# Kernel tuning notes

Hardware: AMD Instinct MI355X
Metric: run time of the kernel (lower is better)

Reference implementation:

```python
import jax, jax.numpy as jnp
import numpy as np

EMBED = 2048
HEADS = 16
HEAD_DIM = EMBED // HEADS


def setup_inputs() -> dict:
    key = jax.random.key(0)
    ks = jax.random.split(key, 9)
    s = 1.0 / np.sqrt(EMBED)
    inp = {"x": jax.random.normal(ks[0], (2, 2048, EMBED), dtype=jnp.float32)}
    for i, name in enumerate(["q", "k", "v", "o"]):
        inp[f"W{name}"] = jax.random.uniform(ks[1 + 2 * i], (EMBED, EMBED), dtype=jnp.float32, minval=-s, maxval=s)
        inp[f"b{name}"] = jax.random.uniform(ks[2 + 2 * i], (EMBED,), dtype=jnp.float32, minval=-s, maxval=s)
    return inp


def reference(x, Wq, bq, Wk, bk, Wv, bv, Wo, bo):
    B, S, E = x.shape
    def split_heads(t):
        return t.reshape(B, S, HEADS, HEAD_DIM).transpose(0, 2, 1, 3)  # [B,H,S,D]
    q = split_heads(x @ Wq.T + bq)
    k = split_heads(x @ Wk.T + bk)
    v = split_heads(x @ Wv.T + bv)
    scale = 1.0 / np.sqrt(HEAD_DIM)
    scores = jnp.einsum("bhqd,bhkd->bhqk", q, k) * scale  # [B,H,S,S]
    causal = jnp.tril(jnp.ones((S, S), dtype=bool))
    scores = jnp.where(causal[None, None], scores, -jnp.inf)
    attn = jax.nn.softmax(scores, axis=-1)
    out = jnp.einsum("bhqk,bhkd->bhqd", attn, v)  # [B,H,S,D]
    out = out.transpose(0, 2, 1, 3).reshape(B, S, E)
    return out @ Wo.T + bo
```

## Files before the change

kernel.cpp:

```cpp
#include <hip/hip_runtime.h>

typedef unsigned short u16;
typedef unsigned int u32;
typedef __attribute__((ext_vector_type(8))) short bf16x8;
typedef __attribute__((ext_vector_type(4))) float f32x4;

#define MFMA(a, b, c) __builtin_amdgcn_mfma_f32_16x16x32_bf16((a), (b), (c), 0, 0, 0)

__device__ inline u16 f2bf(float f) {
  u32 u = __float_as_uint(f);
  u = (u + 0x7fffu + ((u >> 16) & 1u)) >> 16;
  return (u16)u;
}

__device__ inline void gld16(u16* lds, const u16* g) {
  __builtin_amdgcn_global_load_lds((const __attribute__((address_space(1))) void*)g,
                                   (__attribute__((address_space(3))) void*)lds,
                                   16, 0, 0);
}

__global__ __launch_bounds__(256) void cvt_all(const float* __restrict__ x,
                                               const float* __restrict__ wa,
                                               const float* __restrict__ wb,
                                               const float* __restrict__ wc,
                                               const float* __restrict__ wd,
                                               uint2* __restrict__ dst) {
  int i = blockIdx.x * 256 + threadIdx.x;
  const float* s;
  int off;
  if (i < 2097152) {
    s = x; off = i;
  } else {
    int j = i - 2097152;
    int which = j >> 20;
    off = j & 1048575;
    s = (which == 0) ? wa : (which == 1) ? wb : (which == 2) ? wc : wd;
  }
  float4 f = ((const float4*)s)[off];
  u32 lo = (u32)f2bf(f.x) | ((u32)f2bf(f.y) << 16);
  u32 hi = (u32)f2bf(f.z) | ((u32)f2bf(f.w) << 16);
  dst[i] = make_uint2(lo, hi);
}

__device__ inline void gemm_core(const u16* __restrict__ A, const u16* __restrict__ W,
                                 u16* As, u16* Bs, int m0, int n0, f32x4 acc[4][4]) {
  const int K = 2048;
  const int NT = 64;
  int t = threadIdx.x, w = t >> 6, l = t & 63;
  int wr = (w >> 1) * 64, wc = (w & 1) * 64;
  int fr = l & 15, fg = l >> 4;
  int r0 = t >> 2;
  int r1 = 64 + r0;
  int c00 = (t & 3) ^ ((r0 >> 1) & 3);
  int c01 = (t & 3) ^ ((r1 >> 1) & 3);
  const u16* gA = A + (size_t)m0 * K;
  const u16* gB = W + (size_t)n0 * K;
  size_t a0 = (size_t)r0 * K + c00 * 8;
  size_t a1 = (size_t)r1 * K + c01 * 8;
#pragma unroll
  for (int p = 0; p < 2; ++p) {
    u16* sa = As + p * 4096;
    u16* sb = Bs + p * 4096;
    int kk = p * 32;
    gld16(sa + w * 512, gA + a0 + kk);
    gld16(sa + 2048 + w * 512, gA + a1 + kk);
    gld16(sb + w * 512, gB + a0 + kk);
    gld16(sb + 2048 + w * 512, gB + a1 + kk);
  }
  for (int kt = 0; kt < NT; ++kt) {
    int kt2 = (kt + 2 < NT) ? (kt + 2) : (NT - 1);
    u16* sa = As + ((kt + 2) & 3) * 4096;
    u16* sb = Bs + ((kt + 2) & 3) * 4096;
    int kk = kt2 * 32;
    gld16(sa + w * 512, gA + a0 + kk);
    gld16(sa + 2048 + w * 512, gA + a1 + kk);
    gld16(sb + w * 512, gB + a0 + kk);
    gld16(sb + 2048 + w * 512, gB + a1 + kk);
    asm volatile("s_waitcnt vmcnt(8)\n\ts_barrier" ::: "memory");
    const u16* ca = As + (kt & 3) * 4096;
    const u16* cb = Bs + (kt & 3) * 4096;
    bf16x8 af[4], bfv[4];
#pragma unroll
    for (int i = 0; i < 4; ++i) {
      int ar = wr + i * 16 + fr;
      af[i] = *(const bf16x8*)&ca[ar * 32 + ((fg ^ ((ar >> 1) & 3)) << 3)];
    }
#pragma unroll
    for (int i = 0; i < 4; ++i) {
      int br = wc + i * 16 + fr;
      bfv[i] = *(const bf16x8*)&cb[br * 32 + ((fg ^ ((br >> 1) & 3)) << 3)];
    }
    __builtin_amdgcn_s_setprio(1);
#pragma unroll
    for (int mi = 0; mi < 4; ++mi)
#pragma unroll
      for (int ni = 0; ni < 4; ++ni)
        acc[mi][ni] = MFMA(af[mi], bfv[ni], acc[mi][ni]);
    __builtin_amdgcn_s_setprio(0);
  }
}

__global__ __launch_bounds__(512, 2) void qk_gemm(
    const u16* __restrict__ X, const u16* __restrict__ Wq, const u16* __restrict__ Wk,
    const float* __restrict__ bq, const float* __restrict__ bk, u16* __restrict__ Qo,
    u16* __restrict__ Ko) {
  __shared__ __attribute__((aligned(16))) u16 As[32768];
  __shared__ __attribute__((aligned(16))) u16 Bs[32768];
  const int K = 2048, NT = 64;
  int which = blockIdx.x >> 3;
  int n0 = (blockIdx.x & 7) * 256;
  int m0 = blockIdx.y * 256;
  const u16* W = (which == 0) ? Wq : Wk;
  const float* bias = (which == 0) ? bq : bk;
  u16* out = (which == 0) ? Qo : Ko;
  float scale = (which == 0) ? 0.08838834764831845f : 1.0f;
  int t = threadIdx.x, w = t >> 6, l = t & 63;
  int wm = w >> 2, wn = w & 3;
  int fr = l & 15, fg = l >> 4;
  int r0 = t >> 2;
  int c0 = (t & 3) ^ ((r0 >> 1) & 3);
  const u16* gA = X + (size_t)m0 * K;
  const u16* gB = W + (size_t)n0 * K;
  size_t a0 = (size_t)r0 * K + c0 * 8;
  size_t a1 = a0 + (size_t)128 * K;
  f32x4 zero4 = {0.f, 0.f, 0.f, 0.f};
  f32x4 acc[8][4];
#pragma unroll
  for (int i = 0; i < 8; ++i)
#pragma unroll
    for (int j = 0; j < 4; ++j) acc[i][j] = zero4;
#pragma unroll
  for (int p = 0; p < 2; ++p) {
    u16* sa = As + p * 8192;
    u16* sb = Bs + p * 8192;
    int kk = p * 32;
    gld16(sa + w * 512, gA + a0 + kk);
    gld16(sa + 4096 + w * 512, gA + a1 + kk);
    gld16(sb + w * 512, gB + a0 + kk);
    gld16(sb + 4096 + w * 512, gB + a1 + kk);
  }
  for (int kt = 0; kt < NT; ++kt) {
    int kt2 = (kt + 2 < NT) ? (kt + 2) : (NT - 1);
    u16* sa = As + ((kt + 2) & 3) * 8192;
    u16* sb = Bs + ((kt + 2) & 3) * 8192;
    int kk = kt2 * 32;
    gld16(sa + w * 512, gA + a0 + kk);
    gld16(sa + 4096 + w * 512, gA + a1 + kk);
    gld16(sb + w * 512, gB + a0 + kk);
    gld16(sb + 4096 + w * 512, gB + a1 + kk);
    asm volatile("s_waitcnt vmcnt(8)\n\ts_barrier" ::: "memory");
    const u16* ca = As + (kt & 3) * 8192;
    const u16* cb = Bs + (kt & 3) * 8192;
    bf16x8 af[8], bfv[4];
#pragma unroll
    for (int i = 0; i < 8; ++i) {
      int ar = wm * 128 + i * 16 + fr;
      af[i] = *(const bf16x8*)&ca[ar * 32 + ((fg ^ ((ar >> 1) & 3)) << 3)];
    }
#pragma unroll
    for (int i = 0; i < 4; ++i) {
      int br = wn * 64 + i * 16 + fr;
      bfv[i] = *(const bf16x8*)&cb[br * 32 + ((fg ^ ((br >> 1) & 3)) << 3)];
    }
    __builtin_amdgcn_s_setprio(1);
#pragma unroll
    for (int mi = 0; mi < 8; ++mi)
#pragma unroll
      for (int ni = 0; ni < 4; ++ni)
        acc[mi][ni] = MFMA(af[mi], bfv[ni], acc[mi][ni]);
    __builtin_amdgcn_s_setprio(0);
  }
#pragma unroll
  for (int mi = 0; mi < 8; ++mi) {
#pragma unroll
    for (int ni = 0; ni < 4; ++ni) {
      int row = m0 + wm * 128 + mi * 16 + (l >> 4) * 4;
      int col = n0 + wn * 64 + ni * 16 + (l & 15);
      float bb = bias[col];
      int h = col >> 7, d = col & 127;
#pragma unroll
      for (int i = 0; i < 4; ++i) {
        int m = row + i;
        int b = m >> 11, s = m & 2047;
        float v = (acc[mi][ni][i] + bb) * scale;
        out[(((size_t)b * 16 + h) * 2048 + s) * 128 + d] = f2bf(v);
      }
    }
  }
}

__global__ __launch_bounds__(256, 2) void v_gemm(const u16* __restrict__ X,
                                                 const u16* __restrict__ Wv,
                                                 const float* __restrict__ bv,
                                                 u16* __restrict__ Vo) {
  __shared__ __attribute__((aligned(16))) u16 As[16384];
  __shared__ __attribute__((aligned(16))) u16 Bs[16384];
  int n0 = blockIdx.x * 128, m0 = blockIdx.y * 128;
  f32x4 zero4 = {0.f, 0.f, 0.f, 0.f};
  f32x4 acc[4][4];
#pragma unroll
  for (int i = 0; i < 4; ++i)
#pragma unroll
    for (int j = 0; j < 4; ++j) acc[i][j] = zero4;
  gemm_core(X, Wv, As, Bs, m0, n0, acc);
  int t = threadIdx.x, w = t >> 6, l = t & 63;
  int wr = (w >> 1) * 64, wc = (w & 1) * 64;
#pragma unroll
  for (int mi = 0; mi < 4; ++mi) {
#pragma unroll
    for (int ni = 0; ni < 4; ++ni) {
      int row = m0 + wr + mi * 16 + (l >> 4) * 4;
      int col = n0 + wc + ni * 16 + (l & 15);
      float bb = bv[col];
      int h = col >> 7, d = col & 127;
      int b = row >> 11, s = row & 2047;
      u32 p0 = (u32)f2bf(acc[mi][ni][0] + bb) | ((u32)f2bf(acc[mi][ni][1] + bb) << 16);
      u32 p1 = (u32)f2bf(acc[mi][ni][2] + bb) | ((u32)f2bf(acc[mi][ni][3] + bb) << 16);
      *(uint2*)&Vo[((size_t)(b * 16 + h) * 128 + d) * 2048 + s] = make_uint2(p0, p1);
    }
  }
}

__global__ __launch_bounds__(256, 2) void oproj_gemm(const u16* __restrict__ A,
                                                     const u16* __restrict__ W,
                                                     const float* __restrict__ bias,
                                                     float* __restrict__ out) {
  __shared__ __attribute__((aligned(16))) u16 As[16384];
  __shared__ __attribute__((aligned(16))) u16 Bs[16384];
  int n0 = blockIdx.x * 128, m0 = blockIdx.y * 128;
  f32x4 zero4 = {0.f, 0.f, 0.f, 0.f};
  f32x4 acc[4][4];
#pragma unroll
  for (int i = 0; i < 4; ++i)
#pragma unroll
    for (int j = 0; j < 4; ++j) acc[i][j] = zero4;
  gemm_core(A, W, As, Bs, m0, n0, acc);
  int t = threadIdx.x, w = t >> 6, l = t & 63;
  int wr = (w >> 1) * 64, wc = (w & 1) * 64;
#pragma unroll
  for (int mi = 0; mi < 4; ++mi) {
#pragma unroll
    for (int ni = 0; ni < 4; ++ni) {
      int row = m0 + wr + mi * 16 + (l >> 4) * 4;
      int col = n0 + wc + ni * 16 + (l & 15);
      float bb = bias[col];
#pragma unroll
      for (int i = 0; i < 4; ++i) out[(size_t)(row + i) * 2048 + col] = acc[mi][ni][i] + bb;
    }
  }
}

__global__ __launch_bounds__(512, 4) void attn_fwd(const u16* __restrict__ Q,
                                                   const u16* __restrict__ K,
                                                   const u16* __restrict__ Vt,
                                                   u16* __restrict__ AO) {
  __shared__ __attribute__((aligned(16))) u16 Ks[16384];
  __shared__ __attribute__((aligned(16))) u16 Vts[16384];
  __shared__ __attribute__((aligned(16))) u16 Pl[8192];
  const int D = 128;
  int b3 = blockIdx.x;
  int bh = b3 & 31;
  int xq = b3 >> 5;
  int qt = (xq < 8) ? (15 - xq) : (xq - 8);
  int t = threadIdx.x, w = t >> 6, l = t & 63, g = l >> 4, c = l & 15;
  size_t base = (size_t)bh * 2048 * 128;
  const u16* Vbh = Vt + base;
  int q0 = qt * 128;
  int qrw = q0 + w * 16;
  bf16x8 qf[4];
  {
    const u16* qp = Q + base + (size_t)(qrw + c) * D + g * 8;
#pragma unroll
    for (int ks = 0; ks < 4; ++ks) qf[ks] = *(const bf16x8*)(qp + ks * 32);
  }
  f32x4 zero4 = {0.f, 0.f, 0.f, 0.f};
  f32x4 oacc[8];
#pragma unroll
  for (int i = 0; i < 8; ++i) oacc[i] = zero4;
  f32x4 lacc = zero4;
  bf16x8 ones;
#pragma unroll
  for (int i = 0; i < 8; ++i) ones[i] = (short)0x3F80;
  float mrow[4];
#pragma unroll
  for (int i = 0; i < 4; ++i) mrow[i] = -1e30f;
  char* pw = (char*)(Pl + w * 1024);
  int ktmax = 2 * qt + 1;
#define STAGE_TILE(BUF, KV0)                                                          \
  {                                                                                   \
    _Pragma("unroll") for (int i = 0; i < 2; ++i) {                                   \
      int row = i * 32 + w * 4 + (l >> 4);                                            \
      int cc = (l & 15) ^ (row & 7);                                                  \
      gld16(Ks + (BUF)*8192 + i * 4096 + w * 512,                                     \
            K + base + (size_t)((KV0) + row) * D + cc * 8);                           \
    }                                                                                 \
    _Pragma("unroll") for (int i = 0; i < 2; ++i) {                                   \
      int vr = i * 64 + w * 8 + (l >> 3);                                             \
      int vslot = (l & 7) ^ ((l >> 3) & 7);                                           \
      gld16(Vts + (BUF)*8192 + i * 4096 + w * 512,                                    \
            Vbh + (size_t)vr * 2048 + (KV0) + vslot * 8);                             \
    }                                                                                 \
  }
  STAGE_TILE(0, 0)
  for (int kt = 0; kt <= ktmax; ++kt) {
    int kv0 = kt * 64;
    int ktn = (kt + 1 <= ktmax) ? (kt + 1) : ktmax;
    STAGE_TILE((kt + 1) & 1, ktn * 64)
    asm volatile("s_waitcnt vmcnt(4)\n\ts_barrier" ::: "memory");
    const u16* Kb = Ks + (kt & 1) * 8192;
    const u16* Vb2 = Vts + (kt & 1) * 8192;
    if (kv0 <= qrw + 15) {
      f32x4 sacc[4];
#pragma unroll
      for (int n = 0; n < 4; ++n) sacc[n] = zero4;
#pragma unroll
      for (int ks = 0; ks < 4; ++ks) {
#pragma unroll
        for (int n = 0; n < 4; ++n) {
          int row = n * 16 + c;
          bf16x8 kf = *(const bf16x8*)&Kb[row * 128 + (((ks * 4 + g) ^ (c & 7)) << 3)];
          sacc[n] = MFMA(qf[ks], kf, sacc[n]);
        }
      }
      float sc[4][4];
#pragma unroll
      for (int n = 0; n < 4; ++n)
#pragma unroll
        for (int i = 0; i < 4; ++i) sc[n][i] = sacc[n][i];
      if (kv0 + 63 > qrw) {
#pragma unroll
        for (int n = 0; n < 4; ++n) {
          int kv = kv0 + n * 16 + c;
#pragma unroll
          for (int i = 0; i < 4; ++i)
            if (kv > qrw + g * 4 + i) sc[n][i] = -1e30f;
        }
      }
      float tmax[4];
#pragma unroll
      for (int i = 0; i < 4; ++i)
        tmax[i] = fmaxf(fmaxf(sc[0][i], sc[1][i]), fmaxf(sc[2][i], sc[3][i]));
#pragma unroll
      for (int x = 1; x < 16; x <<= 1)
#pragma unroll
        for (int i = 0; i < 4; ++i) tmax[i] = fmaxf(tmax[i], __shfl_xor(tmax[i], x));
      float corr[4];
#pragma unroll
      for (int i = 0; i < 4; ++i) {
        float mn = fmaxf(mrow[i], tmax[i]);
        corr[i] = __expf(mrow[i] - mn);
        mrow[i] = mn;
      }
#pragma unroll
      for (int i = 0; i < 4; ++i) lacc[i] *= corr[i];
#pragma unroll
      for (int nf = 0; nf < 8; ++nf)
#pragma unroll
        for (int i = 0; i < 4; ++i) oacc[nf][i] *= corr[i];
      float ps[4][4];
#pragma unroll
      for (int n = 0; n < 4; ++n)
#pragma unroll
        for (int i = 0; i < 4; ++i) ps[n][i] = __expf(sc[n][i] - mrow[i]);
#pragma unroll
      for (int n = 0; n < 4; ++n)
#pragma unroll
        for (int i = 0; i < 4; ++i) {
          int row = g * 4 + i;
          *(u16*)(pw + row * 128 + ((n * 32 + c * 2) ^ ((row & 7) << 4))) = f2bf(ps[n][i]);
        }
#pragma unroll
      for (int ks = 0; ks < 2; ++ks) {
        bf16x8 pf = *(const bf16x8*)(pw + c * 128 + ((ks * 64 + g * 16) ^ ((c & 7) << 4)));
        lacc = MFMA(pf, ones, lacc);
#pragma unroll
        for (int nf = 0; nf < 8; ++nf) {
          bf16x8 vf = *(const bf16x8*)&Vb2[(nf * 16 + c) * 64 + (((ks * 4 + g) ^ (c & 7)) << 3)];
          oacc[nf] = MFMA(pf, vf, oacc[nf]);
        }
      }
    }
    __syncthreads();
  }
  int b = bh >> 4, h = bh & 15;
#pragma unroll
  for (int nf = 0; nf < 8; ++nf) {
    int d = h * 128 + nf * 16 + c;
#pragma unroll
    for (int i = 0; i < 4; ++i) {
      int q = qrw + g * 4 + i;
      AO[((size_t)b * 2048 + q) * 2048 + d] = f2bf(oacc[nf][i] / lacc[i]);
    }
  }
}

extern "C" void kernel_launch(void* const* d_in, const int* in_sizes, int n_in,
                              void* d_out, int out_size, void* d_ws, size_t ws_size,
                              hipStream_t stream) {
  const float* x = (const float*)d_in[0];
  const float* Wq = (const float*)d_in[1];
  const float* bq = (const float*)d_in[2];
  const float* Wk = (const float*)d_in[3];
  const float* bk = (const float*)d_in[4];
  const float* Wv = (const float*)d_in[5];
  const float* bv = (const float*)d_in[6];
  const float* Wo = (const float*)d_in[7];
  const float* bo = (const float*)d_in[8];
  float* out = (float*)d_out;

  u16* xb = (u16*)d_ws;
  u16* Wqb = xb + 8388608;
  u16* Wkb = Wqb + 4194304;
  u16* Wvb = Wkb + 4194304;
  u16* Wob = Wvb + 4194304;
  u16* Qb = Wob + 4194304;
  u16* Kb = Qb + 8388608;
  u16* Vb = Kb + 8388608;
  u16* AOb = xb;

  cvt_all<<<24576, 256, 0, stream>>>(x, Wq, Wk, Wv, Wo, (uint2*)d_ws);
  qk_gemm<<<dim3(16, 16), 512, 0, stream>>>(xb, Wqb, Wkb, bq, bk, Qb, Kb);
  v_gemm<<<dim3(16, 32), 256, 0, stream>>>(xb, Wvb, bv, Vb);
  attn_fwd<<<512, 512, 0, stream>>>(Qb, Kb, Vb, AOb);
  oproj_gemm<<<dim3(16, 32), 256, 0, stream>>>(AOb, Wob, bo, out);
}
```

Baseline: 259.1 us.

## Use single-buffered 128-wide KV tiles in attention instead of double-buffered 64

The attention loop now stages 128-key K and V tiles into the whole LDS region, replacing two alternating 64-key buffers. This halves the number of loop iterations, barriers and online-softmax rescales per key. In exchange it drops prefetching of the next tile, so global loads no longer overlap with MFMA work and each iteration waits for all loads. The P matrix is written and consumed in two halves to reuse the per-warp P buffer.

```diff
diff --git a/kernel.cpp b/kernel.cpp
--- a/kernel.cpp
+++ b/kernel.cpp
@@ -285,51 +285,44 @@
 #pragma unroll
   for (int i = 0; i < 4; ++i) mrow[i] = -1e30f;
   char* pw = (char*)(Pl + w * 1024);
-  int ktmax = 2 * qt + 1;
-#define STAGE_TILE(BUF, KV0)                                                          \
-  {                                                                                   \
-    _Pragma("unroll") for (int i = 0; i < 2; ++i) {                                   \
-      int row = i * 32 + w * 4 + (l >> 4);                                            \
-      int cc = (l & 15) ^ (row & 7);                                                  \
-      gld16(Ks + (BUF)*8192 + i * 4096 + w * 512,                                     \
-            K + base + (size_t)((KV0) + row) * D + cc * 8);                           \
-    }                                                                                 \
-    _Pragma("unroll") for (int i = 0; i < 2; ++i) {                                   \
-      int vr = i * 64 + w * 8 + (l >> 3);                                             \
-      int vslot = (l & 7) ^ ((l >> 3) & 7);                                           \
-      gld16(Vts + (BUF)*8192 + i * 4096 + w * 512,                                    \
-            Vbh + (size_t)vr * 2048 + (KV0) + vslot * 8);                             \
-    }                                                                                 \
-  }
-  STAGE_TILE(0, 0)
-  for (int kt = 0; kt <= ktmax; ++kt) {
-    int kv0 = kt * 64;
-    int ktn = (kt + 1 <= ktmax) ? (kt + 1) : ktmax;
-    STAGE_TILE((kt + 1) & 1, ktn * 64)
-    asm volatile("s_waitcnt vmcnt(4)\n\ts_barrier" ::: "memory");
-    const u16* Kb = Ks + (kt & 1) * 8192;
-    const u16* Vb2 = Vts + (kt & 1) * 8192;
+  for (int kt = 0; kt <= qt; ++kt) {
+    int kv0 = kt * 128;
+    __syncthreads();
+#pragma unroll
+    for (int i = 0; i < 4; ++i) {
+      int row = i * 32 + w * 4 + (l >> 4);
+      int cc = (l & 15) ^ (row & 7);
+      gld16(Ks + i * 4096 + w * 512, K + base + (size_t)(kv0 + row) * D + cc * 8);
+    }
+#pragma unroll
+    for (int i = 0; i < 4; ++i) {
+      int vr = i * 32 + w * 4 + (l >> 4);
+      int cc = (l & 15) ^ (vr & 7);
+      gld16(Vts + i * 4096 + w * 512, Vbh + (size_t)vr * 2048 + kv0 + cc * 8);
+    }
+    asm volatile("s_waitcnt vmcnt(0)" ::: "memory");
+    __syncthreads();
     if (kv0 <= qrw + 15) {
-      f32x4 sacc[4];
-#pragma unroll
-      for (int n = 0; n < 4; ++n) sacc[n] = zero4;
+      f32x4 sacc[8];
+#pragma unroll
+      for (int n = 0; n < 8; ++n) sacc[n] = zero4;
 #pragma unroll
       for (int ks = 0; ks < 4; ++ks) {
 #pragma unroll
-        for (int n = 0; n < 4; ++n) {
+        for (int n = 0; n < 8; ++n) {
           int row = n * 16 + c;
-          bf16x8 kf = *(const bf16x8*)&Kb[row * 128 + (((ks * 4 + g) ^ (c & 7)) << 3)];
+          bf16x8 kf = *(const bf16x8*)&Ks[row * 128 + (((ks * 4 + g) ^ (c & 7)) << 3)];
           sacc[n] = MFMA(qf[ks], kf, sacc[n]);
         }
       }
-      float sc[4][4];
-#pragma unroll
-      for (int n = 0; n < 4; ++n)
+      float sc[8][4];
+#pragma unroll
+      for (int n = 0; n < 8; ++n)
 #pragma unroll
         for (int i = 0; i < 4; ++i) sc[n][i] = sacc[n][i];
-      if (kv0 + 63 > qrw) {
-#pragma unroll
-        for (int n = 0; n < 4; ++n) {
+      if (kv0 + 127 > qrw) {
+#pragma unroll
+        for (int n = 0; n < 8; ++n) {
           int kv = kv0 + n * 16 + c;
 #pragma unroll
           for (int i = 0; i < 4; ++i)
@@ -338,8 +331,11 @@
       }
       float tmax[4];
 #pragma unroll
-      for (int i = 0; i < 4; ++i)
-        tmax[i] = fmaxf(fmaxf(sc[0][i], sc[1][i]), fmaxf(sc[2][i], sc[3][i]));
+      for (int i = 0; i < 4; ++i) {
+        float m01 = fmaxf(sc[0][i], sc[1][i]), m23 = fmaxf(sc[2][i], sc[3][i]);
+        float m45 = fmaxf(sc[4][i], sc[5][i]), m67 = fmaxf(sc[6][i], sc[7][i]);
+        tmax[i] = fmaxf(fmaxf(m01, m23), fmaxf(m45, m67));
+      }
 #pragma unroll
       for (int x = 1; x < 16; x <<= 1)
 #pragma unroll
@@ -357,30 +353,34 @@
       for (int nf = 0; nf < 8; ++nf)
 #pragma unroll
         for (int i = 0; i < 4; ++i) oacc[nf][i] *= corr[i];
-      float ps[4][4];
-#pragma unroll
-      for (int n = 0; n < 4; ++n)
-#pragma unroll
-        for (int i = 0; i < 4; ++i) ps[n][i] = __expf(sc[n][i] - mrow[i]);
-#pragma unroll
-      for (int n = 0; n < 4; ++n)
-#pragma unroll
-        for (int i = 0; i < 4; ++i) {
-          int row = g * 4 + i;
-          *(u16*)(pw + row * 128 + ((n * 32 + c * 2) ^ ((row & 7) << 4))) = f2bf(ps[n][i]);
+#pragma unroll
+      for (int n = 0; n < 8; ++n)
+#pragma unroll
+        for (int i = 0; i < 4; ++i) sc[n][i] = __expf(sc[n][i] - mrow[i]);
+#pragma unroll
+      for (int hf = 0; hf < 2; ++hf) {
+#pragma unroll
+        for (int n4 = 0; n4 < 4; ++n4)
+#pragma unroll
+          for (int i = 0; i < 4; ++i) {
+            int row = g * 4 + i;
+            *(u16*)(pw + row * 128 + ((n4 * 32 + c * 2) ^ ((row & 7) << 4))) =
+                f2bf(sc[hf * 4 + n4][i]);
+          }
+#pragma unroll
+        for (int ks2 = 0; ks2 < 2; ++ks2) {
+          int ks = hf * 2 + ks2;
+          bf16x8 pf = *(const bf16x8*)(pw + c * 128 + ((ks2 * 64 + g * 16) ^ ((c & 7) << 4)));
+          lacc = MFMA(pf, ones, lacc);
+#pragma unroll
+          for (int nf = 0; nf < 8; ++nf) {
+            bf16x8 vf =
+                *(const bf16x8*)&Vts[(nf * 16 + c) * 128 + (((ks * 4 + g) ^ (c & 7)) << 3)];
+            oacc[nf] = MFMA(pf, vf, oacc[nf]);
+          }
         }
-#pragma unroll
-      for (int ks = 0; ks < 2; ++ks) {
-        bf16x8 pf = *(const bf16x8*)(pw + c * 128 + ((ks * 64 + g * 16) ^ ((c & 7) << 4)));
-        lacc = MFMA(pf, ones, lacc);
-#pragma unroll
-        for (int nf = 0; nf < 8; ++nf) {
-          bf16x8 vf = *(const bf16x8*)&Vb2[(nf * 16 + c) * 64 + (((ks * 4 + g) ^ (c & 7)) << 3)];
-          oacc[nf] = MFMA(pf, vf, oacc[nf]);
-        }
-      }
-    }
-    __syncthreads();
+      }
+    }
   }
   int b = bh >> 4, h = bh & 15;
 #pragma unroll
```

Result: slower. 268.0 us (+3.4%).
